# Performance work log

Hardware: AMD Instinct MI355X
Metric: run time of the kernel (lower is better)

## Reference

```python
import jax, jax.numpy as jnp
import numpy as np

B, S, HID = 2, 2048, 2048
NH, NKV, HD = 32, 8, 64
N_REP = NH // NKV
SCALING = HD ** -0.5
NEG_INF = -1e9


def rotate_half(x):
    x1, x2 = x[..., : x.shape[-1] // 2], x[..., x.shape[-1] // 2 :]
    return jnp.concatenate((-x2, x1), axis=-1)


def setup_inputs() -> dict:
    key = jax.random.key(0)
    ks = jax.random.split(key, 5)
    hidden_states = jax.random.normal(ks[0], (B, S, HID), dtype=jnp.float32)
    # real RoPE tables, theta=10000
    inv_freq = 1.0 / (10000.0 ** (jnp.arange(0, HD, 2, dtype=jnp.float32) / HD))
    freqs = jnp.arange(S, dtype=jnp.float32)[:, None] * inv_freq[None, :]  # [S, HD/2]
    emb = jnp.concatenate((freqs, freqs), axis=-1)  # [S, HD]
    cos = jnp.broadcast_to(jnp.cos(emb)[None], (B, S, HD))
    sin = jnp.broadcast_to(jnp.sin(emb)[None], (B, S, HD))
    # additive causal mask [B, 1, S, S]
    causal = jnp.tril(jnp.ones((S, S), dtype=bool))
    attention_mask = jnp.where(causal, 0.0, NEG_INF).astype(jnp.float32)
    attention_mask = jnp.broadcast_to(attention_mask[None, None], (B, 1, S, S))
    std = 0.02
    Wq = jax.random.normal(ks[1], (NH * HD, HID), dtype=jnp.float32) * std
    Wk = jax.random.normal(ks[2], (NKV * HD, HID), dtype=jnp.float32) * std
    Wv = jax.random.normal(ks[3], (NKV * HD, HID), dtype=jnp.float32) * std
    Wo = jax.random.normal(ks[4], (HID, NH * HD), dtype=jnp.float32) * std
    return {"hidden_states": hidden_states, "cos": cos, "sin": sin,
            "attention_mask": attention_mask, "Wq": Wq, "Wk": Wk, "Wv": Wv, "Wo": Wo}


def reference(hidden_states, cos, sin, attention_mask, Wq, Wk, Wv, Wo):
    b, s, _ = hidden_states.shape
    # projections (nn.Linear: y = x @ W.T), split heads -> [b, h, s, d]
    q = jnp.einsum("bsh,oh->bso", hidden_states, Wq).reshape(b, s, NH, HD).transpose(0, 2, 1, 3)
    k = jnp.einsum("bsh,oh->bso", hidden_states, Wk).reshape(b, s, NKV, HD).transpose(0, 2, 1, 3)
    v = jnp.einsum("bsh,oh->bso", hidden_states, Wv).reshape(b, s, NKV, HD).transpose(0, 2, 1, 3)
    # RoPE (cos/sin unsqueezed at dim 1)
    c, sn = cos[:, None], sin[:, None]
    q = q * c + rotate_half(q) * sn
    k = k * c + rotate_half(k) * sn
    # GQA repeat_kv
    k = jnp.repeat(k, N_REP, axis=1)
    v = jnp.repeat(v, N_REP, axis=1)
    # eager attention: QK^T -> +mask -> fp32 softmax -> V
    logits = jnp.einsum("bhqd,bhkd->bhqk", q, k) * SCALING + attention_mask
    attn_weights = jax.nn.softmax(logits.astype(jnp.float32), axis=-1).astype(q.dtype)
    attn_out = jnp.einsum("bhqk,bhkd->bhqd", attn_weights, v)
    attn_out = attn_out.transpose(0, 2, 1, 3).reshape(b, s, NH * HD)
    out = jnp.einsum("bso,ho->bsh", attn_out, Wo)
    return out, attn_weights
```

## Files before the change

kernel.cpp:

```cpp
#include <hip/hip_runtime.h>
#include <hip/hip_bf16.h>


typedef __bf16 bf16;
typedef bf16 bf16x8 __attribute__((ext_vector_type(8)));
typedef bf16 bf16x4 __attribute__((ext_vector_type(4)));
typedef float f32x4 __attribute__((ext_vector_type(4)));

#define B_   2
#define S_   2048
#define HID_ 2048
#define NH_  32
#define NKV_ 8
#define HD_  64
#define TOK_ (B_*S_)
#define QKVN 3072

__device__ __forceinline__ void gl_lds16(const bf16* g, bf16* l) {
  __builtin_amdgcn_global_load_lds(
      (const __attribute__((address_space(1))) unsigned int*)(g),
      (__attribute__((address_space(3))) unsigned int*)(l), 16, 0, 0);
}

__global__ __launch_bounds__(256) void cast_f32_bf16(const float* __restrict__ in,
                                                     bf16* __restrict__ out, int n4) {
  int i = blockIdx.x * 256 + threadIdx.x;
  if (i >= n4) return;
  f32x4 v = ((const f32x4*)in)[i];
  bf16x4 o;
  o[0] = (bf16)v[0]; o[1] = (bf16)v[1]; o[2] = (bf16)v[2]; o[3] = (bf16)v[3];
  ((bf16x4*)out)[i] = o;
}

__global__ __launch_bounds__(256) void cast_wqkv(const float* __restrict__ wq,
                                                 const float* __restrict__ wk,
                                                 const float* __restrict__ wv,
                                                 bf16* __restrict__ dst) {
  int i = blockIdx.x * 256 + threadIdx.x;
  const float* src; int off;
  if (i < 1048576)      { src = wq; off = i; }
  else if (i < 1310720) { src = wk; off = i - 1048576; }
  else                  { src = wv; off = i - 1310720; }
  f32x4 v = ((const f32x4*)src)[off];
  bf16x4 o;
  o[0] = (bf16)v[0]; o[1] = (bf16)v[1]; o[2] = (bf16)v[2]; o[3] = (bf16)v[3];
  ((bf16x4*)dst)[i] = o;
}

template<bool OUT_F32>
__global__ __launch_bounds__(256) void gemm_bt(const bf16* __restrict__ A,
                                               const bf16* __restrict__ Bm,
                                               void* __restrict__ Cout,
                                               int M, int N, int K) {
  __shared__ __align__(16) bf16 As[128 * 32];
  __shared__ __align__(16) bf16 Bs[128 * 32];
  const int tid  = threadIdx.x;
  const int wave = tid >> 6, lane = tid & 63;

  const int nwg = (int)(gridDim.x * gridDim.y);
  const int bid = (int)(blockIdx.y * gridDim.x + blockIdx.x);
  const int swz = (bid & 7) * (nwg >> 3) + (bid >> 3);
  const int bx = swz % (int)gridDim.x, by = swz / (int)gridDim.x;

  const int bm = by * 128, bn = bx * 128;
  const int wm = (wave >> 1) * 64, wn = (wave & 1) * 64;
  const int fr = lane & 15, fg = lane >> 4;

  const int r0   = wave * 32 + (lane >> 2);
  const int scol = (lane & 3) * 8;
  const bf16* ga0 = A  + (size_t)(bm + r0) * K + scol;
  const bf16* ga1 = ga0 + (size_t)16 * K;
  const bf16* gb0 = Bm + (size_t)(bn + r0) * K + scol;
  const bf16* gb1 = gb0 + (size_t)16 * K;
  bf16* lA0 = As + (wave * 32) * 32;
  bf16* lA1 = lA0 + 16 * 32;
  bf16* lB0 = Bs + (wave * 32) * 32;
  bf16* lB1 = lB0 + 16 * 32;

  f32x4 acc[4][4] = {};

  for (int k0 = 0; k0 < K; k0 += 32) {
    gl_lds16(ga0 + k0, lA0);
    gl_lds16(ga1 + k0, lA1);
    gl_lds16(gb0 + k0, lB0);
    gl_lds16(gb1 + k0, lB1);
    __syncthreads();
    bf16x8 af[4], bfv[4];
#pragma unroll
    for (int i = 0; i < 4; ++i) {
      af[i]  = *(const bf16x8*)&As[(wm + i * 16 + fr) * 32 + fg * 8];
      bfv[i] = *(const bf16x8*)&Bs[(wn + i * 16 + fr) * 32 + fg * 8];
    }
#pragma unroll
    for (int i = 0; i < 4; ++i)
#pragma unroll
      for (int j = 0; j < 4; ++j)
        acc[i][j] = __builtin_amdgcn_mfma_f32_16x16x32_bf16(af[i], bfv[j], acc[i][j], 0, 0, 0);
    __syncthreads();
  }

#pragma unroll
  for (int i = 0; i < 4; ++i)
#pragma unroll
    for (int j = 0; j < 4; ++j)
#pragma unroll
      for (int r = 0; r < 4; ++r) {
        int row = bm + wm + i * 16 + fg * 4 + r;
        int col = bn + wn + j * 16 + fr;
        float v = acc[i][j][r];
        if (OUT_F32) __builtin_nontemporal_store(v, &((float*)Cout)[(size_t)row * N + col]);
        else         ((bf16*)Cout)[(size_t)row * N + col] = (bf16)v;
      }
}

__global__ __launch_bounds__(256) void rope_fused(bf16* __restrict__ qkv,
                                                  const float* __restrict__ cosp,
                                                  const float* __restrict__ sinp) {
  const int t = blockIdx.x;
  const int tid = threadIdx.x;
  const int d = tid & 31, g = tid >> 5;
  const float c = cosp[t * 64 + d];
  const float s = sinp[t * 64 + d];
  bf16* row = qkv + (size_t)t * QKVN;
#pragma unroll
  for (int i = 0; i < 4; ++i) {
    bf16* p = row + (g + i * 8) * 64 + d;
    float x1 = (float)p[0], x2 = (float)p[32];
    p[0]  = (bf16)(x1 * c - x2 * s);
    p[32] = (bf16)(x2 * c + x1 * s);
  }
  bf16* p = row + 2048 + g * 64 + d;
  float x1 = (float)p[0], x2 = (float)p[32];
  p[0]  = (bf16)(x1 * c - x2 * s);
  p[32] = (bf16)(x2 * c + x1 * s);
}

__global__ __launch_bounds__(256) void transpose_v(const bf16* __restrict__ v,
                                                   bf16* __restrict__ vT) {
  __shared__ __align__(16) bf16 t[64][72];
  const int bkv = blockIdx.y;
  const int b = bkv >> 3, kv = bkv & 7;
  const int s0 = blockIdx.x * 64;
  const int tid = threadIdx.x;
  const int r = tid >> 3, c = (tid & 7) * 8;
#pragma unroll
  for (int p = 0; p < 2; ++p) {
    int rr = r + p * 32;
    *(bf16x8*)&t[rr][c] = *(const bf16x8*)&v[(size_t)(b * S_ + s0 + rr) * QKVN + kv * 64 + c];
  }
  __syncthreads();
#pragma unroll
  for (int p = 0; p < 2; ++p) {
    int d = r + p * 32;
    bf16x8 o;
#pragma unroll
    for (int j = 0; j < 8; ++j) o[j] = t[c + j][d];
    *(bf16x8*)&vT[((size_t)bkv * 64 + d) * S_ + s0 + c] = o;
  }
}

__global__ __launch_bounds__(256, 4) void attn_kernel(const bf16* __restrict__ qkv,
                                                      const bf16* __restrict__ vT,
                                                      float* __restrict__ attnw,
                                                      bf16* __restrict__ attn_out)
{
  __shared__ __align__(16) bf16 Ks[64][72];
  __shared__ __align__(16) bf16 Vs[64][72];
  __shared__ __align__(16) bf16 Ps[4][16][72];

  const int tid  = threadIdx.x;
  const int wave = tid >> 6, lane = tid & 63;
  const int qt = blockIdx.x;
  const int bh = blockIdx.y;
  const int b = bh >> 5, h = bh & 31, kv = h >> 2;
  const int qLo = qt * 64;
  const int qHi = (31 - qt) * 64;
  const int NT  = 32 - qt;
  const int fr = lane & 15, fg = lane >> 4;
  const int rw = wave * 16;
  const int rt = rw + fg * 4;

  bf16x8 aqL[2], aqH[2];
  {
    const bf16* qp = qkv + (size_t)(b * S_ + qLo + rw + fr) * QKVN + h * 64 + fg * 8;
    aqL[0] = *(const bf16x8*)qp;  aqL[1] = *(const bf16x8*)(qp + 32);
    qp = qkv + (size_t)(b * S_ + qHi + rw + fr) * QKVN + h * 64 + fg * 8;
    aqH[0] = *(const bf16x8*)qp;  aqH[1] = *(const bf16x8*)(qp + 32);
  }

  const int lr = tid >> 2;
  const int lc = (tid & 3) * 16;
  const bf16* kbase = qkv + (size_t)(b * S_) * QKVN + 2048 + kv * 64;
  const bf16* vbase = vT + (size_t)(b * NKV_ + kv) * 64 * S_;
  const bf16* kst = kbase + (size_t)lr * QKVN + lc;
  const bf16* vst = vbase + (size_t)lr * S_ + lc;

  float rsL[4] = {0.f,0.f,0.f,0.f}, rsH[4] = {0.f,0.f,0.f,0.f};
  {
    bf16x8 kr0 = *(const bf16x8*)(kst);
    bf16x8 kr1 = *(const bf16x8*)(kst + 8);
    for (int jt = 0; jt < NT; ++jt) {
      __syncthreads();
      *(bf16x8*)&Ks[lr][lc]     = kr0;
      *(bf16x8*)&Ks[lr][lc + 8] = kr1;
      __syncthreads();
      if (jt + 1 < NT) {
        const bf16* p = kst + (size_t)(jt + 1) * 64 * QKVN;
        kr0 = *(const bf16x8*)(p);
        kr1 = *(const bf16x8*)(p + 8);
      }
      {
        f32x4 acc[4] = {};
#pragma unroll
        for (int nn = 0; nn < 4; ++nn) {
          bf16x8 bk0 = *(const bf16x8*)&Ks[nn*16 + fr][fg*8];
          bf16x8 bk1 = *(const bf16x8*)&Ks[nn*16 + fr][32 + fg*8];
          acc[nn] = __builtin_amdgcn_mfma_f32_16x16x32_bf16(aqH[0], bk0, acc[nn], 0, 0, 0);
          acc[nn] = __builtin_amdgcn_mfma_f32_16x16x32_bf16(aqH[1], bk1, acc[nn], 0, 0, 0);
        }
        if (jt < NT - 1) {
#pragma unroll
          for (int nn = 0; nn < 4; ++nn)
#pragma unroll
            for (int r = 0; r < 4; ++r) rsH[r] += __expf(acc[nn][r] * 0.125f);
        } else {
#pragma unroll
          for (int nn = 0; nn < 4; ++nn)
#pragma unroll
            for (int r = 0; r < 4; ++r)
              if (nn * 16 + fr <= rt + r) rsH[r] += __expf(acc[nn][r] * 0.125f);
        }
      }
      if (jt <= qt) {
        f32x4 acc[4] = {};
#pragma unroll
        for (int nn = 0; nn < 4; ++nn) {
          bf16x8 bk0 = *(const bf16x8*)&Ks[nn*16 + fr][fg*8];
          bf16x8 bk1 = *(const bf16x8*)&Ks[nn*16 + fr][32 + fg*8];
          acc[nn] = __builtin_amdgcn_mfma_f32_16x16x32_bf16(aqL[0], bk0, acc[nn], 0, 0, 0);
          acc[nn] = __builtin_amdgcn_mfma_f32_16x16x32_bf16(aqL[1], bk1, acc[nn], 0, 0, 0);
        }
        if (jt < qt) {
#pragma unroll
          for (int nn = 0; nn < 4; ++nn)
#pragma unroll
            for (int r = 0; r < 4; ++r) rsL[r] += __expf(acc[nn][r] * 0.125f);
        } else {
#pragma unroll
          for (int nn = 0; nn < 4; ++nn)
#pragma unroll
            for (int r = 0; r < 4; ++r)
              if (nn * 16 + fr <= rt + r) rsL[r] += __expf(acc[nn][r] * 0.125f);
        }
      }
    }
  }
#pragma unroll
  for (int r = 0; r < 4; ++r) {
    float v = rsL[r];
    v += __shfl_xor(v, 1); v += __shfl_xor(v, 2);
    v += __shfl_xor(v, 4); v += __shfl_xor(v, 8);
    rsL[r] = 1.0f / v;
    v = rsH[r];
    v += __shfl_xor(v, 1); v += __shfl_xor(v, 2);
    v += __shfl_xor(v, 4); v += __shfl_xor(v, 8);
    rsH[r] = 1.0f / v;
  }

  {
    f32x4 z4 = {0.f, 0.f, 0.f, 0.f};
    const int zLo = (qt + 1) * 64;
    for (int rr = 0; rr < 16; ++rr) {
      size_t base = ((size_t)bh * S_ + qLo + rw + rr) * S_;
      for (int c = zLo + lane * 4; c < S_; c += 256)
        __builtin_nontemporal_store(z4, (f32x4*)&attnw[base + c]);
    }
    const int zHi = NT * 64;
    for (int rr = 0; rr < 16; ++rr) {
      size_t base = ((size_t)bh * S_ + qHi + rw + rr) * S_;
      for (int c = zHi + lane * 4; c < S_; c += 256)
        __builtin_nontemporal_store(z4, (f32x4*)&attnw[base + c]);
    }
  }

  f32x4 oL[4] = {}, oH[4] = {};
  {
    float* awpL = attnw + ((size_t)bh * S_ + qLo + rt) * S_ + fr;
    float* awpH = attnw + ((size_t)bh * S_ + qHi + rt) * S_ + fr;
    bf16x8 kr0 = *(const bf16x8*)(kst);
    bf16x8 kr1 = *(const bf16x8*)(kst + 8);
    bf16x8 vr0 = *(const bf16x8*)(vst);
    bf16x8 vr1 = *(const bf16x8*)(vst + 8);
    for (int jt = 0; jt < NT; ++jt) {
      __syncthreads();
      *(bf16x8*)&Ks[lr][lc]     = kr0;
      *(bf16x8*)&Ks[lr][lc + 8] = kr1;
      *(bf16x8*)&Vs[lr][lc]     = vr0;
      *(bf16x8*)&Vs[lr][lc + 8] = vr1;
      __syncthreads();
      if (jt + 1 < NT) {
        const bf16* p = kst + (size_t)(jt + 1) * 64 * QKVN;
        kr0 = *(const bf16x8*)(p);
        kr1 = *(const bf16x8*)(p + 8);
        p = vst + (size_t)(jt + 1) * 64;
        vr0 = *(const bf16x8*)(p);
        vr1 = *(const bf16x8*)(p + 8);
      }
      {
        f32x4 acc[4] = {};
#pragma unroll
        for (int nn = 0; nn < 4; ++nn) {
          bf16x8 bk0 = *(const bf16x8*)&Ks[nn*16 + fr][fg*8];
          bf16x8 bk1 = *(const bf16x8*)&Ks[nn*16 + fr][32 + fg*8];
          acc[nn] = __builtin_amdgcn_mfma_f32_16x16x32_bf16(aqH[0], bk0, acc[nn], 0, 0, 0);
          acc[nn] = __builtin_amdgcn_mfma_f32_16x16x32_bf16(aqH[1], bk1, acc[nn], 0, 0, 0);
        }
        if (jt < NT - 1) {
#pragma unroll
          for (int nn = 0; nn < 4; ++nn)
#pragma unroll
            for (int r = 0; r < 4; ++r) {
              float pv = __expf(acc[nn][r] * 0.125f) * rsH[r];
              __builtin_nontemporal_store(pv, awpH + (size_t)r * S_ + nn * 16);
              Ps[wave][fg * 4 + r][nn * 16 + fr] = (bf16)pv;
            }
        } else {
#pragma unroll
          for (int nn = 0; nn < 4; ++nn)
#pragma unroll
            for (int r = 0; r < 4; ++r) {
              float pv = (nn * 16 + fr > rt + r) ? 0.f
                         : __expf(acc[nn][r] * 0.125f) * rsH[r];
              __builtin_nontemporal_store(pv, awpH + (size_t)r * S_ + nn * 16);
              Ps[wave][fg * 4 + r][nn * 16 + fr] = (bf16)pv;
            }
        }
        bf16x8 pa0 = *(const bf16x8*)&Ps[wave][fr][fg * 8];
        bf16x8 pa1 = *(const bf16x8*)&Ps[wave][fr][32 + fg * 8];
#pragma unroll
        for (int nn = 0; nn < 4; ++nn) {
          bf16x8 bv0 = *(const bf16x8*)&Vs[nn*16 + fr][fg*8];
          bf16x8 bv1 = *(const bf16x8*)&Vs[nn*16 + fr][32 + fg*8];
          oH[nn] = __builtin_amdgcn_mfma_f32_16x16x32_bf16(pa0, bv0, oH[nn], 0, 0, 0);
          oH[nn] = __builtin_amdgcn_mfma_f32_16x16x32_bf16(pa1, bv1, oH[nn], 0, 0, 0);
        }
        awpH += 64;
      }
      if (jt <= qt) {
        f32x4 acc[4] = {};
#pragma unroll
        for (int nn = 0; nn < 4; ++nn) {
          bf16x8 bk0 = *(const bf16x8*)&Ks[nn*16 + fr][fg*8];
          bf16x8 bk1 = *(const bf16x8*)&Ks[nn*16 + fr][32 + fg*8];
          acc[nn] = __builtin_amdgcn_mfma_f32_16x16x32_bf16(aqL[0], bk0, acc[nn], 0, 0, 0);
          acc[nn] = __builtin_amdgcn_mfma_f32_16x16x32_bf16(aqL[1], bk1, acc[nn], 0, 0, 0);
        }
        if (jt < qt) {
#pragma unroll
          for (int nn = 0; nn < 4; ++nn)
#pragma unroll
            for (int r = 0; r < 4; ++r) {
              float pv = __expf(acc[nn][r] * 0.125f) * rsL[r];
              __builtin_nontemporal_store(pv, awpL + (size_t)r * S_ + nn * 16);
              Ps[wave][fg * 4 + r][nn * 16 + fr] = (bf16)pv;
            }
        } else {
#pragma unroll
          for (int nn = 0; nn < 4; ++nn)
#pragma unroll
            for (int r = 0; r < 4; ++r) {
              float pv = (nn * 16 + fr > rt + r) ? 0.f
                         : __expf(acc[nn][r] * 0.125f) * rsL[r];
              __builtin_nontemporal_store(pv, awpL + (size_t)r * S_ + nn * 16);
              Ps[wave][fg * 4 + r][nn * 16 + fr] = (bf16)pv;
            }
        }
        bf16x8 pa0 = *(const bf16x8*)&Ps[wave][fr][fg * 8];
        bf16x8 pa1 = *(const bf16x8*)&Ps[wave][fr][32 + fg * 8];
#pragma unroll
        for (int nn = 0; nn < 4; ++nn) {
          bf16x8 bv0 = *(const bf16x8*)&Vs[nn*16 + fr][fg*8];
          bf16x8 bv1 = *(const bf16x8*)&Vs[nn*16 + fr][32 + fg*8];
          oL[nn] = __builtin_amdgcn_mfma_f32_16x16x32_bf16(pa0, bv0, oL[nn], 0, 0, 0);
          oL[nn] = __builtin_amdgcn_mfma_f32_16x16x32_bf16(pa1, bv1, oL[nn], 0, 0, 0);
        }
        awpL += 64;
      }
    }
  }

#pragma unroll
  for (int nn = 0; nn < 4; ++nn)
#pragma unroll
    for (int r = 0; r < 4; ++r) {
      int rowL = qLo + rt + r;
      int rowH = qHi + rt + r;
      attn_out[(size_t)(b * S_ + rowL) * (NH_*HD_) + h * 64 + nn * 16 + fr] = (bf16)oL[nn][r];
      attn_out[(size_t)(b * S_ + rowH) * (NH_*HD_) + h * 64 + nn * 16 + fr] = (bf16)oH[nn][r];
    }
}

extern "C" void kernel_launch(void* const* d_in, const int* in_sizes, int n_in,
                              void* d_out, int out_size, void* d_ws, size_t ws_size,
                              hipStream_t stream) {
  const float* hs   = (const float*)d_in[0];
  const float* cosp = (const float*)d_in[1];
  const float* sinp = (const float*)d_in[2];
  const float* Wq = (const float*)d_in[4];
  const float* Wk = (const float*)d_in[5];
  const float* Wv = (const float*)d_in[6];
  const float* Wo = (const float*)d_in[7];

  char* ws = (char*)d_ws;
  bf16* hs_b   = (bf16*)(ws);
  bf16* qkv_b  = (bf16*)(ws + (16u << 20));
  bf16* vT_b   = (bf16*)(ws + (40u << 20));
  bf16* ao_b   = (bf16*)(ws + (44u << 20));
  bf16* Wqkv_b = (bf16*)(ws + (60u << 20));
  bf16* Wo_b   = (bf16*)(ws + (72u << 20));

  float* outp  = (float*)d_out;
  float* attnw = outp + (size_t)TOK_ * HID_;

  cast_f32_bf16<<<(TOK_*HID_/4 + 255)/256, 256, 0, stream>>>(hs, hs_b, TOK_*HID_/4);
  cast_wqkv<<<(1572864 + 255)/256, 256, 0, stream>>>(Wq, Wk, Wv, Wqkv_b);
  cast_f32_bf16<<<(HID_*NH_*HD_/4 + 255)/256, 256, 0, stream>>>(Wo, Wo_b, HID_*NH_*HD_/4);

  gemm_bt<false><<<dim3(QKVN/128, TOK_/128), 256, 0, stream>>>(hs_b, Wqkv_b, qkv_b, TOK_, QKVN, HID_);

  rope_fused<<<TOK_, 256, 0, stream>>>(qkv_b, cosp, sinp);

  transpose_v<<<dim3(S_/64, B_*NKV_), 256, 0, stream>>>(qkv_b + 2560, vT_b);

  attn_kernel<<<dim3(S_/128, B_*NH_), 256, 0, stream>>>(qkv_b, vT_b, attnw, ao_b);

  gemm_bt<true><<<dim3(HID_/128, TOK_/128), 256, 0, stream>>>(ao_b, Wo_b, outp, TOK_, HID_, HID_);
}
```

Baseline: 494.5 us.

## Split attention into row-sum and store kernels with 128-row, 512-thread blocks

Splits the fused attention kernel into two launches. The first computes softmax denominators, writes them to a workspace buffer and zero-fills the masked region. The second recomputes QK^T, writes normalized weights and accumulates PV. Each block now covers 128 query rows per half with 8 waves, and the sums pass double-buffers K in LDS to remove one barrier per tile. The cost is an extra launch and a workspace round trip, halving the grid to 512 blocks, and more per-wave masking branches, which may reduce occupancy or parallelism.

```diff
diff --git a/kernel.cpp b/kernel.cpp
--- a/kernel.cpp
+++ b/kernel.cpp
@@ -159,23 +159,21 @@
   }
 }
 
-__global__ __launch_bounds__(256, 4) void attn_kernel(const bf16* __restrict__ qkv,
-                                                      const bf16* __restrict__ vT,
-                                                      float* __restrict__ attnw,
-                                                      bf16* __restrict__ attn_out)
+__global__ __launch_bounds__(512, 4) void attn_sums(const bf16* __restrict__ qkv,
+                                                    float* __restrict__ rs_buf,
+                                                    float* __restrict__ attnw)
 {
-  __shared__ __align__(16) bf16 Ks[64][72];
-  __shared__ __align__(16) bf16 Vs[64][72];
-  __shared__ __align__(16) bf16 Ps[4][16][72];
+  __shared__ __align__(16) bf16 Ks2[2][64][72];
 
   const int tid  = threadIdx.x;
   const int wave = tid >> 6, lane = tid & 63;
   const int qt = blockIdx.x;
   const int bh = blockIdx.y;
   const int b = bh >> 5, h = bh & 31, kv = h >> 2;
-  const int qLo = qt * 64;
-  const int qHi = (31 - qt) * 64;
-  const int NT  = 32 - qt;
+  const int qLo = qt * 128;
+  const int qHi = (15 - qt) * 128;
+  const int NT  = 32 - 2 * qt;
+  const int loNT = 2 * qt + 2;
   const int fr = lane & 15, fg = lane >> 4;
   const int rw = wave * 16;
   const int rt = rw + fg * 4;
@@ -188,28 +186,178 @@
     aqH[0] = *(const bf16x8*)qp;  aqH[1] = *(const bf16x8*)(qp + 32);
   }
 
-  const int lr = tid >> 2;
-  const int lc = (tid & 3) * 16;
-  const bf16* kbase = qkv + (size_t)(b * S_) * QKVN + 2048 + kv * 64;
-  const bf16* vbase = vT + (size_t)(b * NKV_ + kv) * 64 * S_;
-  const bf16* kst = kbase + (size_t)lr * QKVN + lc;
-  const bf16* vst = vbase + (size_t)lr * S_ + lc;
+  const int lr = tid >> 3;
+  const int lc = (tid & 7) * 8;
+  const bf16* kst = qkv + (size_t)(b * S_) * QKVN + 2048 + kv * 64
+                        + (size_t)lr * QKVN + lc;
 
   float rsL[4] = {0.f,0.f,0.f,0.f}, rsH[4] = {0.f,0.f,0.f,0.f};
+
+  bf16x8 kr = *(const bf16x8*)(kst);
+  *(bf16x8*)&Ks2[0][lr][lc] = kr;
+  __syncthreads();
+
+  for (int jt = 0; jt < NT; ++jt) {
+    const int cur = jt & 1;
+    if (jt + 1 < NT) kr = *(const bf16x8*)(kst + (size_t)(jt + 1) * 64 * QKVN);
+    const int j0 = jt * 64;
+
+    {
+      const int dj = j0 - qHi;
+      if (dj <= rw + 15) {
+        f32x4 acc[4] = {};
+#pragma unroll
+        for (int nn = 0; nn < 4; ++nn) {
+          bf16x8 bk0 = *(const bf16x8*)&Ks2[cur][nn*16 + fr][fg*8];
+          bf16x8 bk1 = *(const bf16x8*)&Ks2[cur][nn*16 + fr][32 + fg*8];
+          acc[nn] = __builtin_amdgcn_mfma_f32_16x16x32_bf16(aqH[0], bk0, acc[nn], 0, 0, 0);
+          acc[nn] = __builtin_amdgcn_mfma_f32_16x16x32_bf16(aqH[1], bk1, acc[nn], 0, 0, 0);
+        }
+        if (dj + 63 <= rw) {
+#pragma unroll
+          for (int nn = 0; nn < 4; ++nn)
+#pragma unroll
+            for (int r = 0; r < 4; ++r) rsH[r] += __expf(acc[nn][r] * 0.125f);
+        } else {
+#pragma unroll
+          for (int nn = 0; nn < 4; ++nn)
+#pragma unroll
+            for (int r = 0; r < 4; ++r)
+              if (dj + nn * 16 + fr <= rt + r) rsH[r] += __expf(acc[nn][r] * 0.125f);
+        }
+      }
+    }
+    if (jt < loNT) {
+      const int dj = j0 - qLo;
+      if (dj <= rw + 15) {
+        f32x4 acc[4] = {};
+#pragma unroll
+        for (int nn = 0; nn < 4; ++nn) {
+          bf16x8 bk0 = *(const bf16x8*)&Ks2[cur][nn*16 + fr][fg*8];
+          bf16x8 bk1 = *(const bf16x8*)&Ks2[cur][nn*16 + fr][32 + fg*8];
+          acc[nn] = __builtin_amdgcn_mfma_f32_16x16x32_bf16(aqL[0], bk0, acc[nn], 0, 0, 0);
+          acc[nn] = __builtin_amdgcn_mfma_f32_16x16x32_bf16(aqL[1], bk1, acc[nn], 0, 0, 0);
+        }
+        if (dj + 63 <= rw) {
+#pragma unroll
+          for (int nn = 0; nn < 4; ++nn)
+#pragma unroll
+            for (int r = 0; r < 4; ++r) rsL[r] += __expf(acc[nn][r] * 0.125f);
+        } else {
+#pragma unroll
+          for (int nn = 0; nn < 4; ++nn)
+#pragma unroll
+            for (int r = 0; r < 4; ++r)
+              if (dj + nn * 16 + fr <= rt + r) rsL[r] += __expf(acc[nn][r] * 0.125f);
+        }
+      }
+    }
+
+    if (jt + 1 < NT) *(bf16x8*)&Ks2[cur ^ 1][lr][lc] = kr;
+    __syncthreads();
+  }
+
+#pragma unroll
+  for (int r = 0; r < 4; ++r) {
+    float v = rsL[r];
+    v += __shfl_xor(v, 1); v += __shfl_xor(v, 2);
+    v += __shfl_xor(v, 4); v += __shfl_xor(v, 8);
+    if (fr == 0) rs_buf[(size_t)bh * S_ + qLo + rt + r] = 1.0f / v;
+    v = rsH[r];
+    v += __shfl_xor(v, 1); v += __shfl_xor(v, 2);
+    v += __shfl_xor(v, 4); v += __shfl_xor(v, 8);
+    if (fr == 0) rs_buf[(size_t)bh * S_ + qHi + rt + r] = 1.0f / v;
+  }
+
   {
-    bf16x8 kr0 = *(const bf16x8*)(kst);
-    bf16x8 kr1 = *(const bf16x8*)(kst + 8);
-    for (int jt = 0; jt < NT; ++jt) {
-      __syncthreads();
-      *(bf16x8*)&Ks[lr][lc]     = kr0;
-      *(bf16x8*)&Ks[lr][lc + 8] = kr1;
-      __syncthreads();
-      if (jt + 1 < NT) {
-        const bf16* p = kst + (size_t)(jt + 1) * 64 * QKVN;
-        kr0 = *(const bf16x8*)(p);
-        kr1 = *(const bf16x8*)(p + 8);
-      }
-      {
+    f32x4 z4 = {0.f, 0.f, 0.f, 0.f};
+    const int zLo = loNT * 64;
+    for (int rr = 0; rr < 16; ++rr) {
+      size_t base = ((size_t)bh * S_ + qLo + rw + rr) * S_;
+      for (int c = zLo + lane * 4; c < S_; c += 256)
+        __builtin_nontemporal_store(z4, (f32x4*)&attnw[base + c]);
+    }
+    const int zHi = NT * 64;
+    for (int rr = 0; rr < 16; ++rr) {
+      size_t base = ((size_t)bh * S_ + qHi + rw + rr) * S_;
+      for (int c = zHi + lane * 4; c < S_; c += 256)
+        __builtin_nontemporal_store(z4, (f32x4*)&attnw[base + c]);
+    }
+  }
+}
+
+__global__ __launch_bounds__(512, 4) void attn_store(const bf16* __restrict__ qkv,
+                                                     const bf16* __restrict__ vT,
+                                                     const float* __restrict__ rs_buf,
+                                                     float* __restrict__ attnw,
+                                                     bf16* __restrict__ attn_out)
+{
+  __shared__ __align__(16) bf16 Ks[64][72];
+  __shared__ __align__(16) bf16 Vs[64][72];
+  __shared__ __align__(16) bf16 Ps[8][16][72];
+
+  const int tid  = threadIdx.x;
+  const int wave = tid >> 6, lane = tid & 63;
+  const int qt = blockIdx.x;
+  const int bh = blockIdx.y;
+  const int b = bh >> 5, h = bh & 31, kv = h >> 2;
+  const int qLo = qt * 128;
+  const int qHi = (15 - qt) * 128;
+  const int NT  = 32 - 2 * qt;
+  const int loNT = 2 * qt + 2;
+  const int fr = lane & 15, fg = lane >> 4;
+  const int rw = wave * 16;
+  const int rt = rw + fg * 4;
+
+  bf16x8 aqL[2], aqH[2];
+  {
+    const bf16* qp = qkv + (size_t)(b * S_ + qLo + rw + fr) * QKVN + h * 64 + fg * 8;
+    aqL[0] = *(const bf16x8*)qp;  aqL[1] = *(const bf16x8*)(qp + 32);
+    qp = qkv + (size_t)(b * S_ + qHi + rw + fr) * QKVN + h * 64 + fg * 8;
+    aqH[0] = *(const bf16x8*)qp;  aqH[1] = *(const bf16x8*)(qp + 32);
+  }
+
+  float rsL[4], rsH[4];
+#pragma unroll
+  for (int r = 0; r < 4; ++r) {
+    rsL[r] = rs_buf[(size_t)bh * S_ + qLo + rt + r];
+    rsH[r] = rs_buf[(size_t)bh * S_ + qHi + rt + r];
+  }
+
+  const int lr = tid >> 3;
+  const int lc = (tid & 7) * 8;
+  const bf16* kst = qkv + (size_t)(b * S_) * QKVN + 2048 + kv * 64
+                        + (size_t)lr * QKVN + lc;
+  const bf16* vst = vT + (size_t)(b * NKV_ + kv) * 64 * S_ + (size_t)lr * S_ + lc;
+
+  float* awpL = attnw + ((size_t)bh * S_ + qLo + rt) * S_ + fr;
+  float* awpH = attnw + ((size_t)bh * S_ + qHi + rt) * S_ + fr;
+
+  f32x4 oL[4] = {}, oH[4] = {};
+
+  bf16x8 kr = *(const bf16x8*)(kst);
+  bf16x8 vr = *(const bf16x8*)(vst);
+
+  for (int jt = 0; jt < NT; ++jt) {
+    const int j0 = jt * 64;
+    __syncthreads();
+    *(bf16x8*)&Ks[lr][lc] = kr;
+    *(bf16x8*)&Vs[lr][lc] = vr;
+    __syncthreads();
+    if (jt + 1 < NT) {
+      kr = *(const bf16x8*)(kst + (size_t)(jt + 1) * 64 * QKVN);
+      vr = *(const bf16x8*)(vst + (size_t)(jt + 1) * 64);
+    }
+
+    {
+      const int dj = j0 - qHi;
+      if (dj > rw + 15) {
+#pragma unroll
+        for (int nn = 0; nn < 4; ++nn)
+#pragma unroll
+          for (int r = 0; r < 4; ++r)
+            __builtin_nontemporal_store(0.f, awpH + (size_t)r * S_ + nn * 16);
+      } else {
         f32x4 acc[4] = {};
 #pragma unroll
         for (int nn = 0; nn < 4; ++nn) {
@@ -218,104 +366,7 @@
           acc[nn] = __builtin_amdgcn_mfma_f32_16x16x32_bf16(aqH[0], bk0, acc[nn], 0, 0, 0);
           acc[nn] = __builtin_amdgcn_mfma_f32_16x16x32_bf16(aqH[1], bk1, acc[nn], 0, 0, 0);
         }
-        if (jt < NT - 1) {
-#pragma unroll
-          for (int nn = 0; nn < 4; ++nn)
-#pragma unroll
-            for (int r = 0; r < 4; ++r) rsH[r] += __expf(acc[nn][r] * 0.125f);
-        } else {
-#pragma unroll
-          for (int nn = 0; nn < 4; ++nn)
-#pragma unroll
-            for (int r = 0; r < 4; ++r)
-              if (nn * 16 + fr <= rt + r) rsH[r] += __expf(acc[nn][r] * 0.125f);
-        }
-      }
-      if (jt <= qt) {
-        f32x4 acc[4] = {};
-#pragma unroll
-        for (int nn = 0; nn < 4; ++nn) {
-          bf16x8 bk0 = *(const bf16x8*)&Ks[nn*16 + fr][fg*8];
-          bf16x8 bk1 = *(const bf16x8*)&Ks[nn*16 + fr][32 + fg*8];
-          acc[nn] = __builtin_amdgcn_mfma_f32_16x16x32_bf16(aqL[0], bk0, acc[nn], 0, 0, 0);
-          acc[nn] = __builtin_amdgcn_mfma_f32_16x16x32_bf16(aqL[1], bk1, acc[nn], 0, 0, 0);
-        }
-        if (jt < qt) {
-#pragma unroll
-          for (int nn = 0; nn < 4; ++nn)
-#pragma unroll
-            for (int r = 0; r < 4; ++r) rsL[r] += __expf(acc[nn][r] * 0.125f);
-        } else {
-#pragma unroll
-          for (int nn = 0; nn < 4; ++nn)
-#pragma unroll
-            for (int r = 0; r < 4; ++r)
-              if (nn * 16 + fr <= rt + r) rsL[r] += __expf(acc[nn][r] * 0.125f);
-        }
-      }
-    }
-  }
-#pragma unroll
-  for (int r = 0; r < 4; ++r) {
-    float v = rsL[r];
-    v += __shfl_xor(v, 1); v += __shfl_xor(v, 2);
-    v += __shfl_xor(v, 4); v += __shfl_xor(v, 8);
-    rsL[r] = 1.0f / v;
-    v = rsH[r];
-    v += __shfl_xor(v, 1); v += __shfl_xor(v, 2);
-    v += __shfl_xor(v, 4); v += __shfl_xor(v, 8);
-    rsH[r] = 1.0f / v;
-  }
-
-  {
-    f32x4 z4 = {0.f, 0.f, 0.f, 0.f};
-    const int zLo = (qt + 1) * 64;
-    for (int rr = 0; rr < 16; ++rr) {
-      size_t base = ((size_t)bh * S_ + qLo + rw + rr) * S_;
-      for (int c = zLo + lane * 4; c < S_; c += 256)
-        __builtin_nontemporal_store(z4, (f32x4*)&attnw[base + c]);
-    }
-    const int zHi = NT * 64;
-    for (int rr = 0; rr < 16; ++rr) {
-      size_t base = ((size_t)bh * S_ + qHi + rw + rr) * S_;
-      for (int c = zHi + lane * 4; c < S_; c += 256)
-        __builtin_nontemporal_store(z4, (f32x4*)&attnw[base + c]);
-    }
-  }
-
-  f32x4 oL[4] = {}, oH[4] = {};
-  {
-    float* awpL = attnw + ((size_t)bh * S_ + qLo + rt) * S_ + fr;
-    float* awpH = attnw + ((size_t)bh * S_ + qHi + rt) * S_ + fr;
-    bf16x8 kr0 = *(const bf16x8*)(kst);
-    bf16x8 kr1 = *(const bf16x8*)(kst + 8);
-    bf16x8 vr0 = *(const bf16x8*)(vst);
-    bf16x8 vr1 = *(const bf16x8*)(vst + 8);
-    for (int jt = 0; jt < NT; ++jt) {
-      __syncthreads();
-      *(bf16x8*)&Ks[lr][lc]     = kr0;
-      *(bf16x8*)&Ks[lr][lc + 8] = kr1;
-      *(bf16x8*)&Vs[lr][lc]     = vr0;
-      *(bf16x8*)&Vs[lr][lc + 8] = vr1;
-      __syncthreads();
-      if (jt + 1 < NT) {
-        const bf16* p = kst + (size_t)(jt + 1) * 64 * QKVN;
-        kr0 = *(const bf16x8*)(p);
-        kr1 = *(const bf16x8*)(p + 8);
-        p = vst + (size_t)(jt + 1) * 64;
-        vr0 = *(const bf16x8*)(p);
-        vr1 = *(const bf16x8*)(p + 8);
-      }
-      {
-        f32x4 acc[4] = {};
-#pragma unroll
-        for (int nn = 0; nn < 4; ++nn) {
-          bf16x8 bk0 = *(const bf16x8*)&Ks[nn*16 + fr][fg*8];
-          bf16x8 bk1 = *(const bf16x8*)&Ks[nn*16 + fr][32 + fg*8];
-          acc[nn] = __builtin_amdgcn_mfma_f32_16x16x32_bf16(aqH[0], bk0, acc[nn], 0, 0, 0);
-          acc[nn] = __builtin_amdgcn_mfma_f32_16x16x32_bf16(aqH[1], bk1, acc[nn], 0, 0, 0);
-        }
-        if (jt < NT - 1) {
+        if (dj + 63 <= rw) {
 #pragma unroll
           for (int nn = 0; nn < 4; ++nn)
 #pragma unroll
@@ -329,7 +380,7 @@
           for (int nn = 0; nn < 4; ++nn)
 #pragma unroll
             for (int r = 0; r < 4; ++r) {
-              float pv = (nn * 16 + fr > rt + r) ? 0.f
+              float pv = (dj + nn * 16 + fr > rt + r) ? 0.f
                          : __expf(acc[nn][r] * 0.125f) * rsH[r];
               __builtin_nontemporal_store(pv, awpH + (size_t)r * S_ + nn * 16);
               Ps[wave][fg * 4 + r][nn * 16 + fr] = (bf16)pv;
@@ -344,9 +395,18 @@
           oH[nn] = __builtin_amdgcn_mfma_f32_16x16x32_bf16(pa0, bv0, oH[nn], 0, 0, 0);
           oH[nn] = __builtin_amdgcn_mfma_f32_16x16x32_bf16(pa1, bv1, oH[nn], 0, 0, 0);
         }
-        awpH += 64;
       }
-      if (jt <= qt) {
+      awpH += 64;
+    }
+    if (jt < loNT) {
+      const int dj = j0 - qLo;
+      if (dj > rw + 15) {
+#pragma unroll
+        for (int nn = 0; nn < 4; ++nn)
+#pragma unroll
+          for (int r = 0; r < 4; ++r)
+            __builtin_nontemporal_store(0.f, awpL + (size_t)r * S_ + nn * 16);
+      } else {
         f32x4 acc[4] = {};
 #pragma unroll
         for (int nn = 0; nn < 4; ++nn) {
@@ -355,7 +415,7 @@
           acc[nn] = __builtin_amdgcn_mfma_f32_16x16x32_bf16(aqL[0], bk0, acc[nn], 0, 0, 0);
           acc[nn] = __builtin_amdgcn_mfma_f32_16x16x32_bf16(aqL[1], bk1, acc[nn], 0, 0, 0);
         }
-        if (jt < qt) {
+        if (dj + 63 <= rw) {
 #pragma unroll
           for (int nn = 0; nn < 4; ++nn)
 #pragma unroll
@@ -369,7 +429,7 @@
           for (int nn = 0; nn < 4; ++nn)
 #pragma unroll
             for (int r = 0; r < 4; ++r) {
-              float pv = (nn * 16 + fr > rt + r) ? 0.f
+              float pv = (dj + nn * 16 + fr > rt + r) ? 0.f
                          : __expf(acc[nn][r] * 0.125f) * rsL[r];
               __builtin_nontemporal_store(pv, awpL + (size_t)r * S_ + nn * 16);
               Ps[wave][fg * 4 + r][nn * 16 + fr] = (bf16)pv;
@@ -384,8 +444,8 @@
           oL[nn] = __builtin_amdgcn_mfma_f32_16x16x32_bf16(pa0, bv0, oL[nn], 0, 0, 0);
           oL[nn] = __builtin_amdgcn_mfma_f32_16x16x32_bf16(pa1, bv1, oL[nn], 0, 0, 0);
         }
-        awpL += 64;
       }
+      awpL += 64;
     }
   }
 
@@ -418,6 +478,7 @@
   bf16* ao_b   = (bf16*)(ws + (44u << 20));
   bf16* Wqkv_b = (bf16*)(ws + (60u << 20));
   bf16* Wo_b   = (bf16*)(ws + (72u << 20));
+  float* rs_b  = (float*)(ws + (80u << 20));
 
   float* outp  = (float*)d_out;
   float* attnw = outp + (size_t)TOK_ * HID_;
@@ -432,7 +493,9 @@
 
   transpose_v<<<dim3(S_/64, B_*NKV_), 256, 0, stream>>>(qkv_b + 2560, vT_b);
 
-  attn_kernel<<<dim3(S_/128, B_*NH_), 256, 0, stream>>>(qkv_b, vT_b, attnw, ao_b);
+  attn_sums<<<dim3(8, B_*NH_), 512, 0, stream>>>(qkv_b, rs_b, attnw);
+
+  attn_store<<<dim3(8, B_*NH_), 512, 0, stream>>>(qkv_b, vT_b, rs_b, attnw, ao_b);
 
   gemm_bt<true><<<dim3(HID_/128, TOK_/128), 256, 0, stream>>>(ao_b, Wo_b, outp, TOK_, HID_, HID_);
 }
```

Result: slower. 527.2 us (+6.6%).

## Transpose QK^T MFMA operands so each lane stores 16-byte attention-weight vectors

Applied to the files above, without the earlier changes.

Swaps the A/B operands of the QK^T MFMAs so the score tile comes out transposed: each lane holds four consecutive key columns of one query row. The attention-weight stores become 16-byte f32x4 writes instead of scattered scalar nontemporal stores. The row-sum reduction shrinks to one scalar per lane, reduced with two cross-group shuffles. The diagonal masking branches are merged into one select, and the final GEMM's f32 output switches from nontemporal to plain stores.

```diff
diff --git a/kernel.cpp b/kernel.cpp
--- a/kernel.cpp
+++ b/kernel.cpp
@@ -108,7 +108,7 @@
         int row = bm + wm + i * 16 + fg * 4 + r;
         int col = bn + wn + j * 16 + fr;
         float v = acc[i][j][r];
-        if (OUT_F32) __builtin_nontemporal_store(v, &((float*)Cout)[(size_t)row * N + col]);
+        if (OUT_F32) ((float*)Cout)[(size_t)row * N + col] = v;
         else         ((bf16*)Cout)[(size_t)row * N + col] = (bf16)v;
       }
 }
@@ -179,6 +179,7 @@
   const int fr = lane & 15, fg = lane >> 4;
   const int rw = wave * 16;
   const int rt = rw + fg * 4;
+  const int thr = rw + fr;
 
   bf16x8 aqL[2], aqH[2];
   {
@@ -195,7 +196,7 @@
   const bf16* kst = kbase + (size_t)lr * QKVN + lc;
   const bf16* vst = vbase + (size_t)lr * S_ + lc;
 
-  float rsL[4] = {0.f,0.f,0.f,0.f}, rsH[4] = {0.f,0.f,0.f,0.f};
+  float rsL = 0.f, rsH = 0.f;
   {
     bf16x8 kr0 = *(const bf16x8*)(kst);
     bf16x8 kr1 = *(const bf16x8*)(kst + 8);
@@ -215,20 +216,20 @@
         for (int nn = 0; nn < 4; ++nn) {
           bf16x8 bk0 = *(const bf16x8*)&Ks[nn*16 + fr][fg*8];
           bf16x8 bk1 = *(const bf16x8*)&Ks[nn*16 + fr][32 + fg*8];
-          acc[nn] = __builtin_amdgcn_mfma_f32_16x16x32_bf16(aqH[0], bk0, acc[nn], 0, 0, 0);
-          acc[nn] = __builtin_amdgcn_mfma_f32_16x16x32_bf16(aqH[1], bk1, acc[nn], 0, 0, 0);
+          acc[nn] = __builtin_amdgcn_mfma_f32_16x16x32_bf16(bk0, aqH[0], acc[nn], 0, 0, 0);
+          acc[nn] = __builtin_amdgcn_mfma_f32_16x16x32_bf16(bk1, aqH[1], acc[nn], 0, 0, 0);
         }
         if (jt < NT - 1) {
 #pragma unroll
           for (int nn = 0; nn < 4; ++nn)
 #pragma unroll
-            for (int r = 0; r < 4; ++r) rsH[r] += __expf(acc[nn][r] * 0.125f);
+            for (int r = 0; r < 4; ++r) rsH += __expf(acc[nn][r] * 0.125f);
         } else {
 #pragma unroll
           for (int nn = 0; nn < 4; ++nn)
 #pragma unroll
             for (int r = 0; r < 4; ++r)
-              if (nn * 16 + fr <= rt + r) rsH[r] += __expf(acc[nn][r] * 0.125f);
+              if (nn * 16 + fg * 4 + r <= thr) rsH += __expf(acc[nn][r] * 0.125f);
         }
       }
       if (jt <= qt) {
@@ -237,34 +238,31 @@
         for (int nn = 0; nn < 4; ++nn) {
           bf16x8 bk0 = *(const bf16x8*)&Ks[nn*16 + fr][fg*8];
           bf16x8 bk1 = *(const bf16x8*)&Ks[nn*16 + fr][32 + fg*8];
-          acc[nn] = __builtin_amdgcn_mfma_f32_16x16x32_bf16(aqL[0], bk0, acc[nn], 0, 0, 0);
-          acc[nn] = __builtin_amdgcn_mfma_f32_16x16x32_bf16(aqL[1], bk1, acc[nn], 0, 0, 0);
+          acc[nn] = __builtin_amdgcn_mfma_f32_16x16x32_bf16(bk0, aqL[0], acc[nn], 0, 0, 0);
+          acc[nn] = __builtin_amdgcn_mfma_f32_16x16x32_bf16(bk1, aqL[1], acc[nn], 0, 0, 0);
         }
         if (jt < qt) {
 #pragma unroll
           for (int nn = 0; nn < 4; ++nn)
 #pragma unroll
-            for (int r = 0; r < 4; ++r) rsL[r] += __expf(acc[nn][r] * 0.125f);
+            for (int r = 0; r < 4; ++r) rsL += __expf(acc[nn][r] * 0.125f);
         } else {
 #pragma unroll
           for (int nn = 0; nn < 4; ++nn)
 #pragma unroll
             for (int r = 0; r < 4; ++r)
-              if (nn * 16 + fr <= rt + r) rsL[r] += __expf(acc[nn][r] * 0.125f);
-        }
-      }
-    }
-  }
-#pragma unroll
-  for (int r = 0; r < 4; ++r) {
-    float v = rsL[r];
-    v += __shfl_xor(v, 1); v += __shfl_xor(v, 2);
-    v += __shfl_xor(v, 4); v += __shfl_xor(v, 8);
-    rsL[r] = 1.0f / v;
-    v = rsH[r];
-    v += __shfl_xor(v, 1); v += __shfl_xor(v, 2);
-    v += __shfl_xor(v, 4); v += __shfl_xor(v, 8);
-    rsH[r] = 1.0f / v;
+              if (nn * 16 + fg * 4 + r <= thr) rsL += __expf(acc[nn][r] * 0.125f);
+        }
+      }
+    }
+  }
+  {
+    float v = rsL;
+    v += __shfl_xor(v, 16); v += __shfl_xor(v, 32);
+    rsL = 1.0f / v;
+    v = rsH;
+    v += __shfl_xor(v, 16); v += __shfl_xor(v, 32);
+    rsH = 1.0f / v;
   }
 
   {
@@ -285,13 +283,15 @@
 
   f32x4 oL[4] = {}, oH[4] = {};
   {
-    float* awpL = attnw + ((size_t)bh * S_ + qLo + rt) * S_ + fr;
-    float* awpH = attnw + ((size_t)bh * S_ + qHi + rt) * S_ + fr;
+    float* awpL = attnw + ((size_t)bh * S_ + qLo + rw + fr) * S_;
+    float* awpH = attnw + ((size_t)bh * S_ + qHi + rw + fr) * S_;
+    const int cb = fg * 4;
     bf16x8 kr0 = *(const bf16x8*)(kst);
     bf16x8 kr1 = *(const bf16x8*)(kst + 8);
     bf16x8 vr0 = *(const bf16x8*)(vst);
     bf16x8 vr1 = *(const bf16x8*)(vst + 8);
     for (int jt = 0; jt < NT; ++jt) {
+      const int j0 = jt * 64;
       __syncthreads();
       *(bf16x8*)&Ks[lr][lc]     = kr0;
       *(bf16x8*)&Ks[lr][lc + 8] = kr1;
@@ -312,28 +312,20 @@
         for (int nn = 0; nn < 4; ++nn) {
           bf16x8 bk0 = *(const bf16x8*)&Ks[nn*16 + fr][fg*8];
           bf16x8 bk1 = *(const bf16x8*)&Ks[nn*16 + fr][32 + fg*8];
-          acc[nn] = __builtin_amdgcn_mfma_f32_16x16x32_bf16(aqH[0], bk0, acc[nn], 0, 0, 0);
-          acc[nn] = __builtin_amdgcn_mfma_f32_16x16x32_bf16(aqH[1], bk1, acc[nn], 0, 0, 0);
-        }
-        if (jt < NT - 1) {
-#pragma unroll
-          for (int nn = 0; nn < 4; ++nn)
-#pragma unroll
-            for (int r = 0; r < 4; ++r) {
-              float pv = __expf(acc[nn][r] * 0.125f) * rsH[r];
-              __builtin_nontemporal_store(pv, awpH + (size_t)r * S_ + nn * 16);
-              Ps[wave][fg * 4 + r][nn * 16 + fr] = (bf16)pv;
-            }
-        } else {
-#pragma unroll
-          for (int nn = 0; nn < 4; ++nn)
-#pragma unroll
-            for (int r = 0; r < 4; ++r) {
-              float pv = (nn * 16 + fr > rt + r) ? 0.f
-                         : __expf(acc[nn][r] * 0.125f) * rsH[r];
-              __builtin_nontemporal_store(pv, awpH + (size_t)r * S_ + nn * 16);
-              Ps[wave][fg * 4 + r][nn * 16 + fr] = (bf16)pv;
-            }
+          acc[nn] = __builtin_amdgcn_mfma_f32_16x16x32_bf16(bk0, aqH[0], acc[nn], 0, 0, 0);
+          acc[nn] = __builtin_amdgcn_mfma_f32_16x16x32_bf16(bk1, aqH[1], acc[nn], 0, 0, 0);
+        }
+        const bool diag = (jt == NT - 1);
+#pragma unroll
+        for (int nn = 0; nn < 4; ++nn) {
+          f32x4 pv;
+#pragma unroll
+          for (int r = 0; r < 4; ++r) {
+            float e = __expf(acc[nn][r] * 0.125f) * rsH;
+            pv[r] = (diag && (nn * 16 + cb + r > thr)) ? 0.f : e;
+            Ps[wave][fr][nn * 16 + cb + r] = (bf16)pv[r];
+          }
+          *(f32x4*)&awpH[j0 + nn * 16 + cb] = pv;
         }
         bf16x8 pa0 = *(const bf16x8*)&Ps[wave][fr][fg * 8];
         bf16x8 pa1 = *(const bf16x8*)&Ps[wave][fr][32 + fg * 8];
@@ -344,7 +336,6 @@
           oH[nn] = __builtin_amdgcn_mfma_f32_16x16x32_bf16(pa0, bv0, oH[nn], 0, 0, 0);
           oH[nn] = __builtin_amdgcn_mfma_f32_16x16x32_bf16(pa1, bv1, oH[nn], 0, 0, 0);
         }
-        awpH += 64;
       }
       if (jt <= qt) {
         f32x4 acc[4] = {};
@@ -352,28 +343,20 @@
         for (int nn = 0; nn < 4; ++nn) {
           bf16x8 bk0 = *(const bf16x8*)&Ks[nn*16 + fr][fg*8];
           bf16x8 bk1 = *(const bf16x8*)&Ks[nn*16 + fr][32 + fg*8];
-          acc[nn] = __builtin_amdgcn_mfma_f32_16x16x32_bf16(aqL[0], bk0, acc[nn], 0, 0, 0);
-          acc[nn] = __builtin_amdgcn_mfma_f32_16x16x32_bf16(aqL[1], bk1, acc[nn], 0, 0, 0);
-        }
-        if (jt < qt) {
-#pragma unroll
-          for (int nn = 0; nn < 4; ++nn)
-#pragma unroll
-            for (int r = 0; r < 4; ++r) {
-              float pv = __expf(acc[nn][r] * 0.125f) * rsL[r];
-              __builtin_nontemporal_store(pv, awpL + (size_t)r * S_ + nn * 16);
-              Ps[wave][fg * 4 + r][nn * 16 + fr] = (bf16)pv;
-            }
-        } else {
-#pragma unroll
-          for (int nn = 0; nn < 4; ++nn)
-#pragma unroll
-            for (int r = 0; r < 4; ++r) {
-              float pv = (nn * 16 + fr > rt + r) ? 0.f
-                         : __expf(acc[nn][r] * 0.125f) * rsL[r];
-              __builtin_nontemporal_store(pv, awpL + (size_t)r * S_ + nn * 16);
-              Ps[wave][fg * 4 + r][nn * 16 + fr] = (bf16)pv;
-            }
+          acc[nn] = __builtin_amdgcn_mfma_f32_16x16x32_bf16(bk0, aqL[0], acc[nn], 0, 0, 0);
+          acc[nn] = __builtin_amdgcn_mfma_f32_16x16x32_bf16(bk1, aqL[1], acc[nn], 0, 0, 0);
+        }
+        const bool diag = (jt == qt);
+#pragma unroll
+        for (int nn = 0; nn < 4; ++nn) {
+          f32x4 pv;
+#pragma unroll
+          for (int r = 0; r < 4; ++r) {
+            float e = __expf(acc[nn][r] * 0.125f) * rsL;
+            pv[r] = (diag && (nn * 16 + cb + r > thr)) ? 0.f : e;
+            Ps[wave][fr][nn * 16 + cb + r] = (bf16)pv[r];
+          }
+          *(f32x4*)&awpL[j0 + nn * 16 + cb] = pv;
         }
         bf16x8 pa0 = *(const bf16x8*)&Ps[wave][fr][fg * 8];
         bf16x8 pa1 = *(const bf16x8*)&Ps[wave][fr][32 + fg * 8];
@@ -384,7 +367,6 @@
           oL[nn] = __builtin_amdgcn_mfma_f32_16x16x32_bf16(pa0, bv0, oL[nn], 0, 0, 0);
           oL[nn] = __builtin_amdgcn_mfma_f32_16x16x32_bf16(pa1, bv1, oL[nn], 0, 0, 0);
         }
-        awpL += 64;
       }
     }
   }
```

Result: faster. 446.0 us (-9.8%).
